# Optimization experiments

Measured on AMD Instinct MI355X. Metric: run time of the kernel, lower is better.

## Reference

```python
import jax, jax.numpy as jnp
import numpy as np
from jax import lax

T, H, F, E, K = 4096, 1024, 2048, 8, 2

def setup_inputs() -> dict:
    key = jax.random.key(0)
    k1, k2, k3, k4 = jax.random.split(key, 4)
    return {
        "hidden_states": jax.random.normal(k1, (T, H), jnp.float32),
        "gate_w": jax.random.normal(k2, (E, H), jnp.float32) * 0.02,
        "w1": jax.random.normal(k3, (E, 2 * F, H), jnp.float32) * 0.02,  # fused gate+up
        "w2": jax.random.normal(k4, (E, H, F), jnp.float32) * 0.02,      # down proj
        "top_k": K,
    }

def reference(hidden_states, gate_w, w1, w2, top_k):
    tokens = hidden_states.shape[0]
    # Router gate (Linear, no bias)
    router_logits = hidden_states @ gate_w.T                     # [T, E]
    probs = jax.nn.softmax(router_logits.astype(jnp.float32), axis=-1)
    topk_w, topk_idx = lax.top_k(probs, top_k)                   # [T, K]
    topk_w = topk_w / jnp.sum(topk_w, axis=-1, keepdims=True)    # renormalize
    # Dense combine weights [T, E] (zero for unselected experts)
    combine = jnp.zeros_like(probs).at[jnp.arange(tokens)[:, None], topk_idx].add(topk_w)
    combine = combine.astype(hidden_states.dtype)

    def expert_step(acc, ew):
        w1_e, w2_e, c_e = ew                                     # [2F,H], [H,F], [T]
        h = hidden_states @ w1_e.T                               # [T, 2F]
        g, u = jnp.split(h, 2, axis=-1)
        y = (jax.nn.silu(g) * u) @ w2_e.T                        # [T, H]
        return acc + c_e[:, None] * y, None

    acc0 = jnp.zeros_like(hidden_states)
    final_hidden_states, _ = lax.scan(expert_step, acc0, (w1, w2, combine.T))
    return final_hidden_states, router_logits
```

## Files before the change

### kernel.cpp

```cpp
#include <hip/hip_runtime.h>

#define T 4096
#define Hdim 1024
#define Fdim 2048
#define NE 8
#define TOPK 2
#define TK (T*TOPK)

typedef unsigned short ushort_t;
typedef __attribute__((ext_vector_type(8))) short bf16x8;
typedef __attribute__((ext_vector_type(4))) float floatx4;

__device__ __forceinline__ ushort_t f2bf(float f) {
    unsigned u = __float_as_uint(f);
    u += 0x7fff + ((u >> 16) & 1);
    return (ushort_t)(u >> 16);
}
__device__ __forceinline__ uint4 cvt8(const float4 a, const float4 b) {
    uint4 r;
    r.x = (unsigned)f2bf(a.x) | ((unsigned)f2bf(a.y) << 16);
    r.y = (unsigned)f2bf(a.z) | ((unsigned)f2bf(a.w) << 16);
    r.z = (unsigned)f2bf(b.x) | ((unsigned)f2bf(b.y) << 16);
    r.w = (unsigned)f2bf(b.z) | ((unsigned)f2bf(b.w) << 16);
    return r;
}
__device__ __forceinline__ void gld16(const ushort_t* g, short* l) {
    __builtin_amdgcn_global_load_lds((const __attribute__((address_space(1))) void*)g,
                                     (__attribute__((address_space(3))) void*)l, 16, 0, 0);
}

__global__ __launch_bounds__(256) void cvt_kernel(const float* __restrict__ src,
                                                  ushort_t* __restrict__ dst)
{
    long i = (long)blockIdx.x * 256 + threadIdx.x;
    float4 a = *(const float4*)(src + i * 8);
    float4 b = *(const float4*)(src + i * 8 + 4);
    *(uint4*)(dst + i * 8) = cvt8(a, b);
}

__global__ __launch_bounds__(64) void router_kernel(
    const float* __restrict__ hs, const float* __restrict__ gw,
    float* __restrict__ logits_out, ushort_t* __restrict__ hsb,
    int2* __restrict__ choice, float2* __restrict__ cwt, int* __restrict__ counts)
{
    const int t = blockIdx.x;
    const int lane = threadIdx.x;
    if (t == 0 && lane < NE) counts[lane] = 0;

    float hreg[16];
#pragma unroll
    for (int i = 0; i < 16; ++i)
        hreg[i] = hs[(long)t * Hdim + lane + 64 * i];

#pragma unroll
    for (int i = 0; i < 16; ++i)
        hsb[(long)t * Hdim + lane + 64 * i] = f2bf(hreg[i]);

    float acc[NE];
#pragma unroll
    for (int e = 0; e < NE; ++e) {
        float s = 0.f;
#pragma unroll
        for (int i = 0; i < 16; ++i)
            s += hreg[i] * gw[e * Hdim + lane + 64 * i];
#pragma unroll
        for (int off = 32; off > 0; off >>= 1)
            s += __shfl_xor(s, off, 64);
        acc[e] = s;
    }

    if (lane < NE) logits_out[t * NE + lane] = acc[lane];

    if (lane == 0) {
        int i1 = 0;
#pragma unroll
        for (int e = 1; e < NE; ++e) if (acc[e] > acc[i1]) i1 = e;
        int i2 = -1;
#pragma unroll
        for (int e = 0; e < NE; ++e) {
            if (e == i1) continue;
            if (i2 < 0 || acc[e] > acc[i2]) i2 = e;
        }
        float p2 = __expf(acc[i2] - acc[i1]);
        float z  = 1.f + p2;
        choice[t] = make_int2(i1, i2);
        cwt[t]    = make_float2(1.f / z, p2 / z);
    }
}

__global__ __launch_bounds__(256) void scatter_kernel(
    const int2* __restrict__ choice, const float2* __restrict__ cwt,
    int* __restrict__ counts, int* __restrict__ tok_slot, float* __restrict__ tok_wt)
{
    __shared__ int lhist[NE];
    __shared__ int lbase[NE];
    __shared__ int lpos[NE];
    const int tid = threadIdx.x;
    if (tid < NE) { lhist[tid] = 0; lpos[tid] = 0; }
    __syncthreads();

    const int t = blockIdx.x * 256 + tid;
    int2   ch = choice[t];
    float2 wv = cwt[t];
    atomicAdd(&lhist[ch.x], 1);
    atomicAdd(&lhist[ch.y], 1);
    __syncthreads();

    if (tid < NE) lbase[tid] = atomicAdd(&counts[tid], lhist[tid]);
    __syncthreads();

    int p1 = atomicAdd(&lpos[ch.x], 1);
    int p2 = atomicAdd(&lpos[ch.y], 1);
    int o1 = lbase[ch.x] + p1;
    int o2 = lbase[ch.y] + p2;
    tok_slot[ch.x * T + o1] = t * TOPK + 0;
    tok_wt [ch.x * T + o1] = wv.x;
    tok_slot[ch.y * T + o2] = t * TOPK + 1;
    tok_wt [ch.y * T + o2] = wv.y;
}

__global__ __launch_bounds__(256) void gemm1_kernel(
    const ushort_t* __restrict__ hsb, const ushort_t* __restrict__ w1b,
    const int* __restrict__ counts, const int* __restrict__ tok_slot,
    ushort_t* __restrict__ actb)
{
    const int e = blockIdx.z;
    const int cnt = counts[e];
    const int row0 = blockIdx.y * 128;
    if (row0 >= cnt) return;
    const int f0 = blockIdx.x * 64;

    __shared__ short As[128 * 64];
    __shared__ short Bs[128 * 64];
    __shared__ int slotLds[128];

    const int tid = threadIdx.x;
    if (tid < 128) {
        int idx = row0 + tid;
        slotLds[tid] = (idx < cnt) ? tok_slot[e * T + idx] : -1;
    }
    __syncthreads();

    const ushort_t* srcA[4];
    const ushort_t* srcB[4];
#pragma unroll
    for (int i = 0; i < 4; ++i) {
        int ci = i * 256 + tid;
        int r  = ci >> 3;
        int gc = (ci & 7) ^ (r & 7);
        int s  = slotLds[r];
        srcA[i] = hsb + (long)(s >= 0 ? (s >> 1) : 0) * Hdim + gc * 8;
        long frow = (r < 64) ? (long)(f0 + r) : (long)(Fdim + f0 + (r - 64));
        srcB[i] = w1b + ((long)e * 2 * Fdim + frow) * Hdim + gc * 8;
    }

    const int lane = tid & 63;
    const int w = tid >> 6;
    const int wm = (w >> 1) * 64;
    const int wn = (w & 1) * 32;
    const int fr = lane & 15, fg = lane >> 4;
    const int cs0 = (fg ^ (fr & 7)) * 8;
    const int cs1 = ((4 + fg) ^ (fr & 7)) * 8;

    floatx4 accg[4][2] = {};
    floatx4 accu[4][2] = {};

    for (int k0 = 0; k0 < Hdim; k0 += 64) {
        __syncthreads();
#pragma unroll
        for (int i = 0; i < 4; ++i) gld16(srcA[i] + k0, &As[(i * 256 + tid) * 8]);
#pragma unroll
        for (int i = 0; i < 4; ++i) gld16(srcB[i] + k0, &Bs[(i * 256 + tid) * 8]);
        __syncthreads();

#pragma unroll
        for (int kk = 0; kk < 2; ++kk) {
            const int cs = kk ? cs1 : cs0;
            bf16x8 a[4], g[2], u[2];
#pragma unroll
            for (int ms = 0; ms < 4; ++ms)
                a[ms] = *(bf16x8*)&As[(wm + ms * 16 + fr) * 64 + cs];
#pragma unroll
            for (int ns = 0; ns < 2; ++ns) {
                g[ns] = *(bf16x8*)&Bs[(wn + ns * 16 + fr) * 64 + cs];
                u[ns] = *(bf16x8*)&Bs[(64 + wn + ns * 16 + fr) * 64 + cs];
            }
#pragma unroll
            for (int ms = 0; ms < 4; ++ms)
#pragma unroll
                for (int ns = 0; ns < 2; ++ns) {
                    accg[ms][ns] = __builtin_amdgcn_mfma_f32_16x16x32_bf16(a[ms], g[ns], accg[ms][ns], 0, 0, 0);
                    accu[ms][ns] = __builtin_amdgcn_mfma_f32_16x16x32_bf16(a[ms], u[ns], accu[ms][ns], 0, 0, 0);
                }
        }
    }

#pragma unroll
    for (int ms = 0; ms < 4; ++ms)
#pragma unroll
        for (int ns = 0; ns < 2; ++ns)
#pragma unroll
            for (int j = 0; j < 4; ++j) {
                int m = wm + ms * 16 + fg * 4 + j;
                int slot = slotLds[m];
                if (slot >= 0) {
                    int fcol = f0 + wn + ns * 16 + fr;
                    float gv = accg[ms][ns][j];
                    float uv = accu[ms][ns][j];
                    float av = (gv / (1.f + __expf(-gv))) * uv;
                    actb[(long)slot * Fdim + fcol] = f2bf(av);
                }
            }
}

__global__ __launch_bounds__(512) void gemm2_kernel(
    const ushort_t* __restrict__ actb, const ushort_t* __restrict__ w2b,
    const int* __restrict__ counts, const int* __restrict__ tok_slot,
    const float* __restrict__ tok_wt, float* __restrict__ partial)
{
    const int e = blockIdx.z;
    const int cnt = counts[e];
    const int row0 = blockIdx.y * 128;
    if (row0 >= cnt) return;
    const int h0 = blockIdx.x * 128;

    __shared__ short As[128 * 64];
    __shared__ short Bs[128 * 64];
    __shared__ int   slotLds[128];
    __shared__ float wtLds[128];

    const int tid = threadIdx.x;
    if (tid < 128) {
        int idx = row0 + tid;
        bool ok = idx < cnt;
        slotLds[tid] = ok ? tok_slot[e * T + idx] : -1;
        wtLds[tid]   = ok ? tok_wt [e * T + idx] : 0.f;
    }
    __syncthreads();

    const ushort_t* srcA[2];
    const ushort_t* srcB[2];
#pragma unroll
    for (int i = 0; i < 2; ++i) {
        int ci = i * 512 + tid;
        int r  = ci >> 3;
        int gc = (ci & 7) ^ (r & 7);
        int s  = slotLds[r];
        srcA[i] = actb + (long)(s >= 0 ? s : 0) * Fdim + gc * 8;
        srcB[i] = w2b + ((long)e * Hdim + (h0 + r)) * Fdim + gc * 8;
    }

    const int lane = tid & 63;
    const int w = tid >> 6;
    const int wm = (w >> 2) * 64;
    const int wn = (w & 3) * 32;
    const int fr = lane & 15, fg = lane >> 4;
    const int cs0 = (fg ^ (fr & 7)) * 8;
    const int cs1 = ((4 + fg) ^ (fr & 7)) * 8;

    floatx4 acc[4][2] = {};

    for (int k0 = 0; k0 < Fdim; k0 += 64) {
        __syncthreads();
        gld16(srcA[0] + k0, &As[tid * 8]);
        gld16(srcA[1] + k0, &As[(512 + tid) * 8]);
        gld16(srcB[0] + k0, &Bs[tid * 8]);
        gld16(srcB[1] + k0, &Bs[(512 + tid) * 8]);
        __syncthreads();

#pragma unroll
        for (int kk = 0; kk < 2; ++kk) {
            const int cs = kk ? cs1 : cs0;
            bf16x8 a[4], b[2];
#pragma unroll
            for (int ms = 0; ms < 4; ++ms)
                a[ms] = *(bf16x8*)&As[(wm + ms * 16 + fr) * 64 + cs];
#pragma unroll
            for (int ns = 0; ns < 2; ++ns)
                b[ns] = *(bf16x8*)&Bs[(wn + ns * 16 + fr) * 64 + cs];
#pragma unroll
            for (int ms = 0; ms < 4; ++ms)
#pragma unroll
                for (int ns = 0; ns < 2; ++ns)
                    acc[ms][ns] = __builtin_amdgcn_mfma_f32_16x16x32_bf16(a[ms], b[ns], acc[ms][ns], 0, 0, 0);
        }
    }

#pragma unroll
    for (int ms = 0; ms < 4; ++ms)
#pragma unroll
        for (int ns = 0; ns < 2; ++ns)
#pragma unroll
            for (int j = 0; j < 4; ++j) {
                int m = wm + ms * 16 + fg * 4 + j;
                int slot = slotLds[m];
                if (slot >= 0) {
                    int hcol = h0 + wn + ns * 16 + fr;
                    partial[(long)slot * Hdim + hcol] = acc[ms][ns][j] * wtLds[m];
                }
            }
}

__global__ __launch_bounds__(256) void combine_kernel(
    const float* __restrict__ partial, float* __restrict__ out)
{
    long i = (long)blockIdx.x * 256 + threadIdx.x;
    int t  = (int)(i / (Hdim / 4));
    int h4 = (int)(i % (Hdim / 4));
    const float4 p0 = *(const float4*)&partial[(long)(2 * t    ) * Hdim + h4 * 4];
    const float4 p1 = *(const float4*)&partial[(long)(2 * t + 1) * Hdim + h4 * 4];
    float4 s;
    s.x = p0.x + p1.x; s.y = p0.y + p1.y; s.z = p0.z + p1.z; s.w = p0.w + p1.w;
    *(float4*)&out[(long)t * Hdim + h4 * 4] = s;
}

extern "C" void kernel_launch(void* const* d_in, const int* in_sizes, int n_in,
                              void* d_out, int out_size, void* d_ws, size_t ws_size,
                              hipStream_t stream)
{
    const float* hs = (const float*)d_in[0];
    const float* gw = (const float*)d_in[1];
    const float* w1 = (const float*)d_in[2];
    const float* w2 = (const float*)d_in[3];

    float* out        = (float*)d_out;
    float* logits_out = out + (long)T * Hdim;

    char* ws = (char*)d_ws;
    size_t off = 0;
    int* counts = (int*)(ws + off);          off += 256;
    int* tok_slot = (int*)(ws + off);        off += (size_t)NE * T * sizeof(int);
    float* tok_wt = (float*)(ws + off);      off += (size_t)NE * T * sizeof(float);
    off = (off + 255) & ~(size_t)255;
    ushort_t* hsb = (ushort_t*)(ws + off);   off += (size_t)T * Hdim * sizeof(ushort_t);
    off = (off + 255) & ~(size_t)255;
    char* w1region = ws + off;               off += (size_t)NE * 2 * Fdim * Hdim * sizeof(ushort_t);
    ushort_t* w1b = (ushort_t*)w1region;
    ushort_t* w2b = (ushort_t*)w1region;
    float* partial = (float*)(w1region + (size_t)NE * Hdim * Fdim * sizeof(ushort_t));
    off = (off + 255) & ~(size_t)255;
    ushort_t* actb = (ushort_t*)(ws + off);  off += (size_t)TK * Fdim * sizeof(ushort_t);
    int2*   choice = (int2*)actb;
    float2* cwt    = (float2*)((char*)actb + (size_t)T * sizeof(int2));

    const long n8_w1 = (long)NE * 2 * Fdim * Hdim / 8;
    const long n8_w2 = (long)NE * Hdim * Fdim / 8;

    cvt_kernel<<<(int)(n8_w1 / 256), 256, 0, stream>>>(w1, w1b);
    router_kernel<<<T, 64, 0, stream>>>(hs, gw, logits_out, hsb, choice, cwt, counts);
    scatter_kernel<<<T / 256, 256, 0, stream>>>(choice, cwt, counts, tok_slot, tok_wt);
    gemm1_kernel<<<dim3(Fdim / 64, T / 128, NE), 256, 0, stream>>>(hsb, w1b, counts, tok_slot, actb);
    cvt_kernel<<<(int)(n8_w2 / 256), 256, 0, stream>>>(w2, w2b);
    gemm2_kernel<<<dim3(Hdim / 128, T / 128, NE), 512, 0, stream>>>(actb, w2b, counts, tok_slot, tok_wt, partial);
    combine_kernel<<<(int)((long)T * Hdim / 4 / 256), 256, 0, stream>>>(partial, out);
}
```

Before: 433.6 us.

## Enlarge gemm1 tile to 256x128 with double-buffered LDS prefetch

```diff
diff --git a/kernel.cpp b/kernel.cpp
--- a/kernel.cpp
+++ b/kernel.cpp
@@ -119,23 +119,23 @@
     tok_wt [ch.y * T + o2] = wv.y;
 }
 
-__global__ __launch_bounds__(256) void gemm1_kernel(
+__global__ __launch_bounds__(512) void gemm1_kernel(
     const ushort_t* __restrict__ hsb, const ushort_t* __restrict__ w1b,
     const int* __restrict__ counts, const int* __restrict__ tok_slot,
     ushort_t* __restrict__ actb)
 {
     const int e = blockIdx.z;
     const int cnt = counts[e];
-    const int row0 = blockIdx.y * 128;
+    const int row0 = blockIdx.y * 256;
     if (row0 >= cnt) return;
-    const int f0 = blockIdx.x * 64;
-
-    __shared__ short As[128 * 64];
-    __shared__ short Bs[128 * 64];
-    __shared__ int slotLds[128];
+    const int f0 = blockIdx.x * 128;
+
+    __shared__ short As[2][256 * 64];
+    __shared__ short Bs[2][256 * 64];
+    __shared__ int slotLds[256];
 
     const int tid = threadIdx.x;
-    if (tid < 128) {
+    if (tid < 256) {
         int idx = row0 + tid;
         slotLds[tid] = (idx < cnt) ? tok_slot[e * T + idx] : -1;
     }
@@ -145,66 +145,131 @@
     const ushort_t* srcB[4];
 #pragma unroll
     for (int i = 0; i < 4; ++i) {
-        int ci = i * 256 + tid;
+        int ci = i * 512 + tid;
         int r  = ci >> 3;
         int gc = (ci & 7) ^ (r & 7);
         int s  = slotLds[r];
         srcA[i] = hsb + (long)(s >= 0 ? (s >> 1) : 0) * Hdim + gc * 8;
-        long frow = (r < 64) ? (long)(f0 + r) : (long)(Fdim + f0 + (r - 64));
+        long frow = (r < 128) ? (long)(f0 + r) : (long)(Fdim + f0 + (r - 128));
         srcB[i] = w1b + ((long)e * 2 * Fdim + frow) * Hdim + gc * 8;
     }
 
     const int lane = tid & 63;
     const int w = tid >> 6;
     const int wm = (w >> 1) * 64;
-    const int wn = (w & 1) * 32;
+    const int fn = (w & 1) * 64;
     const int fr = lane & 15, fg = lane >> 4;
     const int cs0 = (fg ^ (fr & 7)) * 8;
     const int cs1 = ((4 + fg) ^ (fr & 7)) * 8;
 
-    floatx4 accg[4][2] = {};
-    floatx4 accu[4][2] = {};
-
-    for (int k0 = 0; k0 < Hdim; k0 += 64) {
-        __syncthreads();
-#pragma unroll
-        for (int i = 0; i < 4; ++i) gld16(srcA[i] + k0, &As[(i * 256 + tid) * 8]);
-#pragma unroll
-        for (int i = 0; i < 4; ++i) gld16(srcB[i] + k0, &Bs[(i * 256 + tid) * 8]);
-        __syncthreads();
-
-#pragma unroll
-        for (int kk = 0; kk < 2; ++kk) {
-            const int cs = kk ? cs1 : cs0;
-            bf16x8 a[4], g[2], u[2];
-#pragma unroll
-            for (int ms = 0; ms < 4; ++ms)
-                a[ms] = *(bf16x8*)&As[(wm + ms * 16 + fr) * 64 + cs];
-#pragma unroll
-            for (int ns = 0; ns < 2; ++ns) {
-                g[ns] = *(bf16x8*)&Bs[(wn + ns * 16 + fr) * 64 + cs];
-                u[ns] = *(bf16x8*)&Bs[(64 + wn + ns * 16 + fr) * 64 + cs];
-            }
-#pragma unroll
-            for (int ms = 0; ms < 4; ++ms)
-#pragma unroll
-                for (int ns = 0; ns < 2; ++ns) {
-                    accg[ms][ns] = __builtin_amdgcn_mfma_f32_16x16x32_bf16(a[ms], g[ns], accg[ms][ns], 0, 0, 0);
-                    accu[ms][ns] = __builtin_amdgcn_mfma_f32_16x16x32_bf16(a[ms], u[ns], accu[ms][ns], 0, 0, 0);
-                }
-        }
+    floatx4 accg[4][4] = {};
+    floatx4 accu[4][4] = {};
+
+#pragma unroll
+    for (int i = 0; i < 4; ++i) {
+        gld16(srcA[i], &As[0][(i * 512 + tid) * 8]);
+        gld16(srcB[i], &Bs[0][(i * 512 + tid) * 8]);
+    }
+    __syncthreads();
+
+    const int NT = Hdim / 64;
+    for (int t = 0; t < NT; ++t) {
+        short* Ac = As[t & 1];
+        short* Bc = Bs[t & 1];
+        short* An = As[(t & 1) ^ 1];
+        short* Bn = Bs[(t & 1) ^ 1];
+        const bool pf = (t + 1 < NT);
+        const long k1 = (long)(t + 1) * 64;
+
+        bf16x8 a[4], b[4];
+
+#pragma unroll
+        for (int ms = 0; ms < 4; ++ms)
+            a[ms] = *(const bf16x8*)&Ac[(wm + ms * 16 + fr) * 64 + cs0];
+#pragma unroll
+        for (int ns = 0; ns < 4; ++ns)
+            b[ns] = *(const bf16x8*)&Bc[(fn + ns * 16 + fr) * 64 + cs0];
+        if (pf) {
+            gld16(srcA[0] + k1, &An[(0 * 512 + tid) * 8]);
+            gld16(srcB[0] + k1, &Bn[(0 * 512 + tid) * 8]);
+        }
+        __builtin_amdgcn_s_barrier();
+        __builtin_amdgcn_s_setprio(1);
+#pragma unroll
+        for (int ms = 0; ms < 4; ++ms)
+#pragma unroll
+            for (int ns = 0; ns < 4; ++ns)
+                accg[ms][ns] = __builtin_amdgcn_mfma_f32_16x16x32_bf16(a[ms], b[ns], accg[ms][ns], 0, 0, 0);
+        __builtin_amdgcn_s_setprio(0);
+        __builtin_amdgcn_s_barrier();
+
+#pragma unroll
+        for (int ns = 0; ns < 4; ++ns)
+            b[ns] = *(const bf16x8*)&Bc[(128 + fn + ns * 16 + fr) * 64 + cs0];
+        if (pf) {
+            gld16(srcA[1] + k1, &An[(1 * 512 + tid) * 8]);
+            gld16(srcB[1] + k1, &Bn[(1 * 512 + tid) * 8]);
+        }
+        __builtin_amdgcn_s_barrier();
+        __builtin_amdgcn_s_setprio(1);
+#pragma unroll
+        for (int ms = 0; ms < 4; ++ms)
+#pragma unroll
+            for (int ns = 0; ns < 4; ++ns)
+                accu[ms][ns] = __builtin_amdgcn_mfma_f32_16x16x32_bf16(a[ms], b[ns], accu[ms][ns], 0, 0, 0);
+        __builtin_amdgcn_s_setprio(0);
+        __builtin_amdgcn_s_barrier();
+
+#pragma unroll
+        for (int ms = 0; ms < 4; ++ms)
+            a[ms] = *(const bf16x8*)&Ac[(wm + ms * 16 + fr) * 64 + cs1];
+#pragma unroll
+        for (int ns = 0; ns < 4; ++ns)
+            b[ns] = *(const bf16x8*)&Bc[(fn + ns * 16 + fr) * 64 + cs1];
+        if (pf) {
+            gld16(srcA[2] + k1, &An[(2 * 512 + tid) * 8]);
+            gld16(srcB[2] + k1, &Bn[(2 * 512 + tid) * 8]);
+        }
+        __builtin_amdgcn_s_barrier();
+        __builtin_amdgcn_s_setprio(1);
+#pragma unroll
+        for (int ms = 0; ms < 4; ++ms)
+#pragma unroll
+            for (int ns = 0; ns < 4; ++ns)
+                accg[ms][ns] = __builtin_amdgcn_mfma_f32_16x16x32_bf16(a[ms], b[ns], accg[ms][ns], 0, 0, 0);
+        __builtin_amdgcn_s_setprio(0);
+        __builtin_amdgcn_s_barrier();
+
+#pragma unroll
+        for (int ns = 0; ns < 4; ++ns)
+            b[ns] = *(const bf16x8*)&Bc[(128 + fn + ns * 16 + fr) * 64 + cs1];
+        if (pf) {
+            gld16(srcA[3] + k1, &An[(3 * 512 + tid) * 8]);
+            gld16(srcB[3] + k1, &Bn[(3 * 512 + tid) * 8]);
+        }
+        __builtin_amdgcn_s_barrier();
+        __builtin_amdgcn_s_setprio(1);
+#pragma unroll
+        for (int ms = 0; ms < 4; ++ms)
+#pragma unroll
+            for (int ns = 0; ns < 4; ++ns)
+                accu[ms][ns] = __builtin_amdgcn_mfma_f32_16x16x32_bf16(a[ms], b[ns], accu[ms][ns], 0, 0, 0);
+        __builtin_amdgcn_s_setprio(0);
+        __builtin_amdgcn_sched_barrier(0);
+        asm volatile("s_waitcnt vmcnt(0)" ::: "memory");
+        __builtin_amdgcn_s_barrier();
     }
 
 #pragma unroll
     for (int ms = 0; ms < 4; ++ms)
 #pragma unroll
-        for (int ns = 0; ns < 2; ++ns)
+        for (int ns = 0; ns < 4; ++ns)
 #pragma unroll
             for (int j = 0; j < 4; ++j) {
                 int m = wm + ms * 16 + fg * 4 + j;
                 int slot = slotLds[m];
                 if (slot >= 0) {
-                    int fcol = f0 + wn + ns * 16 + fr;
+                    int fcol = f0 + fn + ns * 16 + fr;
                     float gv = accg[ms][ns][j];
                     float uv = accu[ms][ns][j];
                     float av = (gv / (1.f + __expf(-gv))) * uv;
@@ -349,7 +414,7 @@
     cvt_kernel<<<(int)(n8_w1 / 256), 256, 0, stream>>>(w1, w1b);
     router_kernel<<<T, 64, 0, stream>>>(hs, gw, logits_out, hsb, choice, cwt, counts);
     scatter_kernel<<<T / 256, 256, 0, stream>>>(choice, cwt, counts, tok_slot, tok_wt);
-    gemm1_kernel<<<dim3(Fdim / 64, T / 128, NE), 256, 0, stream>>>(hsb, w1b, counts, tok_slot, actb);
+    gemm1_kernel<<<dim3(Fdim / 128, T / 256, NE), 512, 0, stream>>>(hsb, w1b, counts, tok_slot, actb);
     cvt_kernel<<<(int)(n8_w2 / 256), 256, 0, stream>>>(w2, w2b);
     gemm2_kernel<<<dim3(Hdim / 128, T / 128, NE), 512, 0, stream>>>(actb, w2b, counts, tok_slot, tok_wt, partial);
     combine_kernel<<<(int)((long)T * Hdim / 4 / 256), 256, 0, stream>>>(partial, out);
```

New measurement: 429.7 us. No clear change (-0.9%).

## Fuse fp32-to-bf16 weight conversion into expert GEMM tile loads

Applied to the files above, without the earlier changes.

```diff
diff --git a/kernel.cpp b/kernel.cpp
--- a/kernel.cpp
+++ b/kernel.cpp
@@ -27,15 +27,6 @@
 __device__ __forceinline__ void gld16(const ushort_t* g, short* l) {
     __builtin_amdgcn_global_load_lds((const __attribute__((address_space(1))) void*)g,
                                      (__attribute__((address_space(3))) void*)l, 16, 0, 0);
-}
-
-__global__ __launch_bounds__(256) void cvt_kernel(const float* __restrict__ src,
-                                                  ushort_t* __restrict__ dst)
-{
-    long i = (long)blockIdx.x * 256 + threadIdx.x;
-    float4 a = *(const float4*)(src + i * 8);
-    float4 b = *(const float4*)(src + i * 8 + 4);
-    *(uint4*)(dst + i * 8) = cvt8(a, b);
 }
 
 __global__ __launch_bounds__(64) void router_kernel(
@@ -119,39 +110,47 @@
     tok_wt [ch.y * T + o2] = wv.y;
 }
 
-__global__ __launch_bounds__(256) void gemm1_kernel(
-    const ushort_t* __restrict__ hsb, const ushort_t* __restrict__ w1b,
+__global__ __launch_bounds__(512, 3) void gemm1_kernel(
+    const ushort_t* __restrict__ hsb, const float* __restrict__ w1,
     const int* __restrict__ counts, const int* __restrict__ tok_slot,
     ushort_t* __restrict__ actb)
 {
     const int e = blockIdx.z;
     const int cnt = counts[e];
-    const int row0 = blockIdx.y * 128;
+    const int row0 = blockIdx.y * 256;
     if (row0 >= cnt) return;
     const int f0 = blockIdx.x * 64;
 
-    __shared__ short As[128 * 64];
+    __shared__ short As[256 * 64];
     __shared__ short Bs[128 * 64];
-    __shared__ int slotLds[128];
+    __shared__ int slotLds[256];
 
     const int tid = threadIdx.x;
-    if (tid < 128) {
+    if (tid < 256) {
         int idx = row0 + tid;
         slotLds[tid] = (idx < cnt) ? tok_slot[e * T + idx] : -1;
     }
     __syncthreads();
 
     const ushort_t* srcA[4];
-    const ushort_t* srcB[4];
 #pragma unroll
     for (int i = 0; i < 4; ++i) {
-        int ci = i * 256 + tid;
+        int ci = i * 512 + tid;
         int r  = ci >> 3;
         int gc = (ci & 7) ^ (r & 7);
         int s  = slotLds[r];
         srcA[i] = hsb + (long)(s >= 0 ? (s >> 1) : 0) * Hdim + gc * 8;
+    }
+    const float* srcBf[2];
+    int bDst[2];
+#pragma unroll
+    for (int i = 0; i < 2; ++i) {
+        int ci = i * 512 + tid;
+        int r  = ci >> 3;
+        int gc = (ci & 7) ^ (r & 7);
         long frow = (r < 64) ? (long)(f0 + r) : (long)(Fdim + f0 + (r - 64));
-        srcB[i] = w1b + ((long)e * 2 * Fdim + frow) * Hdim + gc * 8;
+        srcBf[i] = w1 + ((long)e * 2 * Fdim + frow) * Hdim + gc * 8;
+        bDst[i]  = ci * 8;
     }
 
     const int lane = tid & 63;
@@ -168,9 +167,13 @@
     for (int k0 = 0; k0 < Hdim; k0 += 64) {
         __syncthreads();
 #pragma unroll
-        for (int i = 0; i < 4; ++i) gld16(srcA[i] + k0, &As[(i * 256 + tid) * 8]);
-#pragma unroll
-        for (int i = 0; i < 4; ++i) gld16(srcB[i] + k0, &Bs[(i * 256 + tid) * 8]);
+        for (int i = 0; i < 4; ++i) gld16(srcA[i] + k0, &As[(i * 512 + tid) * 8]);
+#pragma unroll
+        for (int i = 0; i < 2; ++i) {
+            float4 x = *(const float4*)(srcBf[i] + k0);
+            float4 y = *(const float4*)(srcBf[i] + k0 + 4);
+            *(uint4*)&Bs[bDst[i]] = cvt8(x, y);
+        }
         __syncthreads();
 
 #pragma unroll
@@ -179,11 +182,11 @@
             bf16x8 a[4], g[2], u[2];
 #pragma unroll
             for (int ms = 0; ms < 4; ++ms)
-                a[ms] = *(bf16x8*)&As[(wm + ms * 16 + fr) * 64 + cs];
+                a[ms] = *(const bf16x8*)&As[(wm + ms * 16 + fr) * 64 + cs];
 #pragma unroll
             for (int ns = 0; ns < 2; ++ns) {
-                g[ns] = *(bf16x8*)&Bs[(wn + ns * 16 + fr) * 64 + cs];
-                u[ns] = *(bf16x8*)&Bs[(64 + wn + ns * 16 + fr) * 64 + cs];
+                g[ns] = *(const bf16x8*)&Bs[(wn + ns * 16 + fr) * 64 + cs];
+                u[ns] = *(const bf16x8*)&Bs[(64 + wn + ns * 16 + fr) * 64 + cs];
             }
 #pragma unroll
             for (int ms = 0; ms < 4; ++ms)
@@ -213,8 +216,8 @@
             }
 }
 
-__global__ __launch_bounds__(512) void gemm2_kernel(
-    const ushort_t* __restrict__ actb, const ushort_t* __restrict__ w2b,
+__global__ __launch_bounds__(512, 4) void gemm2_kernel(
+    const ushort_t* __restrict__ actb, const float* __restrict__ w2,
     const int* __restrict__ counts, const int* __restrict__ tok_slot,
     const float* __restrict__ tok_wt, float* __restrict__ partial)
 {
@@ -239,7 +242,6 @@
     __syncthreads();
 
     const ushort_t* srcA[2];
-    const ushort_t* srcB[2];
 #pragma unroll
     for (int i = 0; i < 2; ++i) {
         int ci = i * 512 + tid;
@@ -247,7 +249,16 @@
         int gc = (ci & 7) ^ (r & 7);
         int s  = slotLds[r];
         srcA[i] = actb + (long)(s >= 0 ? s : 0) * Fdim + gc * 8;
-        srcB[i] = w2b + ((long)e * Hdim + (h0 + r)) * Fdim + gc * 8;
+    }
+    const float* srcBf[2];
+    int bDst[2];
+#pragma unroll
+    for (int i = 0; i < 2; ++i) {
+        int ci = i * 512 + tid;
+        int r  = ci >> 3;
+        int gc = (ci & 7) ^ (r & 7);
+        srcBf[i] = w2 + ((long)e * Hdim + (h0 + r)) * Fdim + gc * 8;
+        bDst[i]  = ci * 8;
     }
 
     const int lane = tid & 63;
@@ -262,10 +273,14 @@
 
     for (int k0 = 0; k0 < Fdim; k0 += 64) {
         __syncthreads();
-        gld16(srcA[0] + k0, &As[tid * 8]);
-        gld16(srcA[1] + k0, &As[(512 + tid) * 8]);
-        gld16(srcB[0] + k0, &Bs[tid * 8]);
-        gld16(srcB[1] + k0, &Bs[(512 + tid) * 8]);
+#pragma unroll
+        for (int i = 0; i < 2; ++i) gld16(srcA[i] + k0, &As[(i * 512 + tid) * 8]);
+#pragma unroll
+        for (int i = 0; i < 2; ++i) {
+            float4 x = *(const float4*)(srcBf[i] + k0);
+            float4 y = *(const float4*)(srcBf[i] + k0 + 4);
+            *(uint4*)&Bs[bDst[i]] = cvt8(x, y);
+        }
         __syncthreads();
 
 #pragma unroll
@@ -274,10 +289,10 @@
             bf16x8 a[4], b[2];
 #pragma unroll
             for (int ms = 0; ms < 4; ++ms)
-                a[ms] = *(bf16x8*)&As[(wm + ms * 16 + fr) * 64 + cs];
+                a[ms] = *(const bf16x8*)&As[(wm + ms * 16 + fr) * 64 + cs];
 #pragma unroll
             for (int ns = 0; ns < 2; ++ns)
-                b[ns] = *(bf16x8*)&Bs[(wn + ns * 16 + fr) * 64 + cs];
+                b[ns] = *(const bf16x8*)&Bs[(wn + ns * 16 + fr) * 64 + cs];
 #pragma unroll
             for (int ms = 0; ms < 4; ++ms)
 #pragma unroll
@@ -334,23 +349,15 @@
     off = (off + 255) & ~(size_t)255;
     ushort_t* hsb = (ushort_t*)(ws + off);   off += (size_t)T * Hdim * sizeof(ushort_t);
     off = (off + 255) & ~(size_t)255;
-    char* w1region = ws + off;               off += (size_t)NE * 2 * Fdim * Hdim * sizeof(ushort_t);
-    ushort_t* w1b = (ushort_t*)w1region;
-    ushort_t* w2b = (ushort_t*)w1region;
-    float* partial = (float*)(w1region + (size_t)NE * Hdim * Fdim * sizeof(ushort_t));
+    ushort_t* actb = (ushort_t*)(ws + off);  off += (size_t)TK * Fdim * sizeof(ushort_t);
     off = (off + 255) & ~(size_t)255;
-    ushort_t* actb = (ushort_t*)(ws + off);  off += (size_t)TK * Fdim * sizeof(ushort_t);
+    float* partial = (float*)(ws + off);     off += (size_t)TK * Hdim * sizeof(float);
     int2*   choice = (int2*)actb;
     float2* cwt    = (float2*)((char*)actb + (size_t)T * sizeof(int2));
 
-    const long n8_w1 = (long)NE * 2 * Fdim * Hdim / 8;
-    const long n8_w2 = (long)NE * Hdim * Fdim / 8;
-
-    cvt_kernel<<<(int)(n8_w1 / 256), 256, 0, stream>>>(w1, w1b);
     router_kernel<<<T, 64, 0, stream>>>(hs, gw, logits_out, hsb, choice, cwt, counts);
     scatter_kernel<<<T / 256, 256, 0, stream>>>(choice, cwt, counts, tok_slot, tok_wt);
-    gemm1_kernel<<<dim3(Fdim / 64, T / 128, NE), 256, 0, stream>>>(hsb, w1b, counts, tok_slot, actb);
-    cvt_kernel<<<(int)(n8_w2 / 256), 256, 0, stream>>>(w2, w2b);
-    gemm2_kernel<<<dim3(Hdim / 128, T / 128, NE), 512, 0, stream>>>(actb, w2b, counts, tok_slot, tok_wt, partial);
+    gemm1_kernel<<<dim3(Fdim / 64, T / 256, NE), 512, 0, stream>>>(hsb, w1, counts, tok_slot, actb);
+    gemm2_kernel<<<dim3(Hdim / 128, T / 128, NE), 512, 0, stream>>>(actb, w2, counts, tok_slot, tok_wt, partial);
     combine_kernel<<<(int)((long)T * Hdim / 4 / 256), 256, 0, stream>>>(partial, out);
 }
```

New measurement: 450.3 us. 3.9% more time.
